# Kernel tuning notes

Hardware: AMD Instinct MI355X
Metric: run time of the kernel (lower is better)

Reference implementation:

```python
import jax, jax.numpy as jnp
import numpy as np

SCALE = 0.125          # feature stride 8
OUT = 7                # roi_align output size
SR = 2                 # sampling_ratio
BBW = (10.0, 10.0, 5.0, 5.0)   # torchvision BoxCoder weights
CLAMP = float(np.log(1000.0 / 16.0))
IMG_H, IMG_W = 800.0, 1088.0


def _bilinear(img, ys, xs):
    # img [C,H,W]; ys,xs [P] -> [C,P]
    C, H, W = img.shape
    y = jnp.clip(ys, 0.0, H - 1.0)
    x = jnp.clip(xs, 0.0, W - 1.0)
    y0 = jnp.floor(y); x0 = jnp.floor(x)
    y0i = y0.astype(jnp.int32); x0i = x0.astype(jnp.int32)
    y1i = jnp.minimum(y0i + 1, H - 1); x1i = jnp.minimum(x0i + 1, W - 1)
    ly = y - y0; lx = x - x0
    flat = img.reshape(C, H * W)
    g = lambda yi, xi: flat[:, yi * W + xi]
    return (g(y0i, x0i) * (1 - ly) * (1 - lx) + g(y0i, x1i) * (1 - ly) * lx
            + g(y1i, x0i) * ly * (1 - lx) + g(y1i, x1i) * ly * lx)


def _roi_align(features, boxes, roi_batch):
    # features [B,C,H,W], boxes [N,4] (image coords), roi_batch [N] -> [N,C,7,7]
    B, C, H, W = features.shape
    P = OUT * SR

    def one(b, box):
        x1, y1, x2, y2 = box[0] * SCALE, box[1] * SCALE, box[2] * SCALE, box[3] * SCALE
        rw = jnp.maximum(x2 - x1, 1.0)
        rh = jnp.maximum(y2 - y1, 1.0)
        bw = rw / OUT; bh = rh / OUT
        off = (jnp.arange(OUT)[:, None] + (jnp.arange(SR)[None, :] + 0.5) / SR).reshape(-1)  # [P]
        ys = y1 + off * bh
        xs = x1 + off * bw
        yy = jnp.repeat(ys, P)   # [P*P], y-major
        xx = jnp.tile(xs, P)
        v = _bilinear(features[b], yy, xx)                   # [C, P*P]
        return v.reshape(C, OUT, SR, OUT, SR).mean(axis=(2, 4))  # avg over samples

    return jax.vmap(one)(roi_batch, boxes)


def _decode(deltas, boxes):
    # deltas [N,K,4], boxes [N,4] -> [N,K,4]
    pw = boxes[:, 2] - boxes[:, 0]
    ph = boxes[:, 3] - boxes[:, 1]
    cx = boxes[:, 0] + 0.5 * pw
    cy = boxes[:, 1] + 0.5 * ph
    dx = deltas[..., 0] / BBW[0]; dy = deltas[..., 1] / BBW[1]
    dw = jnp.minimum(deltas[..., 2] / BBW[2], CLAMP)
    dh = jnp.minimum(deltas[..., 3] / BBW[3], CLAMP)
    pcx = dx * pw[:, None] + cx[:, None]
    pcy = dy * ph[:, None] + cy[:, None]
    pww = jnp.exp(dw) * pw[:, None]
    phh = jnp.exp(dh) * ph[:, None]
    out = jnp.stack([
        jnp.clip(pcx - 0.5 * pww, 0.0, IMG_W),
        jnp.clip(pcy - 0.5 * phh, 0.0, IMG_H),
        jnp.clip(pcx + 0.5 * pww, 0.0, IMG_W),
        jnp.clip(pcy + 0.5 * phh, 0.0, IMG_H),
    ], axis=-1)
    return out


def setup_inputs() -> dict:
    key = jax.random.key(0)
    ks = jax.random.split(key, 12)
    B, C, H, W, N, NC = 2, 256, 100, 136, 1000, 2
    features = jax.random.normal(ks[0], (B, C, H, W), jnp.float32)
    # valid proposal boxes in image coords
    cx = jax.random.uniform(ks[1], (N,)) * IMG_W
    cy = jax.random.uniform(ks[2], (N,)) * IMG_H
    bw = jax.random.uniform(ks[3], (N,)) * 240.0 + 16.0
    bh = jax.random.uniform(ks[4], (N,)) * 240.0 + 16.0
    x1 = jnp.clip(cx - 0.5 * bw, 0.0, IMG_W - 2.0)
    y1 = jnp.clip(cy - 0.5 * bh, 0.0, IMG_H - 2.0)
    x2 = jnp.clip(x1 + bw, x1 + 1.0, IMG_W - 1.0)
    y2 = jnp.clip(y1 + bh, y1 + 1.0, IMG_H - 1.0)
    boxes = jnp.stack([x1, y1, x2, y2], axis=-1).astype(jnp.float32)
    roi_batch = jax.random.randint(ks[5], (N,), 0, B, dtype=jnp.int32)
    D = C * OUT * OUT  # 12544
    HID = 1024
    s = 0.02
    fc1_w = jax.random.normal(ks[6], (D, HID), jnp.float32) * s
    fc1_b = jnp.zeros((HID,), jnp.float32)
    fc2_w = jax.random.normal(ks[7], (HID, HID), jnp.float32) * s
    fc2_b = jnp.zeros((HID,), jnp.float32)
    cls_w = jax.random.normal(ks[8], (HID, NC), jnp.float32) * s
    cls_b = jnp.zeros((NC,), jnp.float32)
    bbox_w = jax.random.normal(ks[9], (HID, NC * 4), jnp.float32) * s
    bbox_b = jnp.zeros((NC * 4,), jnp.float32)
    return {"features": features, "boxes": boxes, "roi_batch": roi_batch,
            "fc1_w": fc1_w, "fc1_b": fc1_b, "fc2_w": fc2_w, "fc2_b": fc2_b,
            "cls_w": cls_w, "cls_b": cls_b, "bbox_w": bbox_w, "bbox_b": bbox_b}


def reference(features, boxes, roi_batch, fc1_w, fc1_b, fc2_w, fc2_b, cls_w, cls_b, bbox_w, bbox_b):
    N = boxes.shape[0]
    feats = _roi_align(features, boxes, roi_batch).reshape(N, -1)  # [N, 12544]
    h = jax.nn.relu(feats @ fc1_w + fc1_b)                         # TwoMLPHead fc6
    h = jax.nn.relu(h @ fc2_w + fc2_b)                             # TwoMLPHead fc7
    scores = jax.nn.softmax(h @ cls_w + cls_b, axis=-1)            # [N, 2]
    deltas = (h @ bbox_w + bbox_b).reshape(N, -1, 4)               # [N, 2, 4]
    dec = _decode(deltas, boxes).reshape(N, -1)                    # [N, 8]
    return jnp.concatenate([dec, scores], axis=-1)                 # [N, 10]
```

## Files before the change

### kernel.cpp

```cpp
#include <hip/hip_runtime.h>
#include <hip/hip_bf16.h>

#define BF16 __hip_bfloat16

typedef __bf16 bf16x8 __attribute__((ext_vector_type(8)));
typedef float floatx4 __attribute__((ext_vector_type(4)));
typedef int intx4 __attribute__((ext_vector_type(4)));

__global__ __launch_bounds__(256) void transpose_all(const float* __restrict__ features,
                                                     const float* __restrict__ fc1_w,
                                                     const float* __restrict__ fc2_w,
                                                     BF16* __restrict__ featT,
                                                     BF16* __restrict__ w1t,
                                                     BF16* __restrict__ w2t) {
    __shared__ float tile[32][33];
    int bid = blockIdx.x;
    const float* ip;
    BF16* op;
    int R, C, cx, cy;
    if (bid < 6800) {
        int z = bid / 3400, r = bid - z * 3400;
        cx = r % 425; cy = r / 425;
        R = 256; C = 13600;
        ip = features + (size_t)z * 256 * 13600;
        op = featT + (size_t)z * 256 * 13600;
    } else if (bid < 19344) {
        int r = bid - 6800;
        cx = r & 31; cy = r >> 5;
        R = 12544; C = 1024;
        ip = fc1_w; op = w1t;
    } else {
        int r = bid - 19344;
        cx = r & 31; cy = r >> 5;
        R = 1024; C = 1024;
        ip = fc2_w; op = w2t;
    }
    int tx = threadIdx.x & 31, ty = threadIdx.x >> 5;
    int r0 = cy << 5, c0 = cx << 5;
#pragma unroll
    for (int i = 0; i < 4; ++i)
        tile[ty + i * 8][tx] = ip[(size_t)(r0 + ty + i * 8) * C + c0 + tx];
    __syncthreads();
#pragma unroll
    for (int i = 0; i < 4; ++i)
        op[(size_t)(c0 + ty + i * 8) * R + r0 + tx] = __float2bfloat16(tile[tx][ty + i * 8]);
}

__global__ __launch_bounds__(256) void roi_align_k(const BF16* __restrict__ featT,
                                                   const float* __restrict__ boxes,
                                                   const int* __restrict__ roi_batch,
                                                   BF16* __restrict__ feats) {
    __shared__ __align__(16) int   s_off[196][4];
    __shared__ __align__(16) float s_w[196][4];
    __shared__ BF16 lbuf[12544];
    int roi = blockIdx.x;
    int t = threadIdx.x;
    BF16* orow = feats + (size_t)roi * 12544;
    if (roi >= 1000) {
        uint4* o4 = (uint4*)orow;
        uint4 z = {0u, 0u, 0u, 0u};
        for (int i = t; i < 1568; i += 256) o4[i] = z;
        return;
    }
    int b = roi_batch[roi];

    if (t < 196) {
        float x1 = boxes[roi * 4 + 0] * 0.125f;
        float y1 = boxes[roi * 4 + 1] * 0.125f;
        float x2 = boxes[roi * 4 + 2] * 0.125f;
        float y2 = boxes[roi * 4 + 3] * 0.125f;
        float bw = fmaxf(x2 - x1, 1.0f) * (1.0f / 7.0f);
        float bh = fmaxf(y2 - y1, 1.0f) * (1.0f / 7.0f);
        int cell = t >> 2, s = t & 3;
        int oy = cell / 7, ox = cell - oy * 7;
        int sy = s >> 1, sx = s & 1;
        float yc = y1 + ((float)oy + ((float)sy + 0.5f) * 0.5f) * bh;
        float xc = x1 + ((float)ox + ((float)sx + 0.5f) * 0.5f) * bw;
        yc = fminf(fmaxf(yc, 0.0f), 99.0f);
        xc = fminf(fmaxf(xc, 0.0f), 135.0f);
        float y0f = floorf(yc), x0f = floorf(xc);
        int y0 = (int)y0f, x0 = (int)x0f;
        int y1i = min(y0 + 1, 99), x1i = min(x0 + 1, 135);
        float ly = yc - y0f, lx = xc - x0f;
        s_w[t][0] = (1.0f - ly) * (1.0f - lx) * 0.25f;
        s_w[t][1] = (1.0f - ly) * lx * 0.25f;
        s_w[t][2] = ly * (1.0f - lx) * 0.25f;
        s_w[t][3] = ly * lx * 0.25f;
        s_off[t][0] = (y0 * 136 + x0) * 256;
        s_off[t][1] = (y0 * 136 + x1i) * 256;
        s_off[t][2] = (y1i * 136 + x0) * 256;
        s_off[t][3] = (y1i * 136 + x1i) * 256;
    }
    __syncthreads();

    int cb = t & 31, g = t >> 5;
    const BF16* fb = featT + (size_t)b * (100 * 136 * 256) + cb * 8;
    int chbase = cb * 8;
    for (int cell = g; cell < 49; cell += 8) {
        float a[8];
#pragma unroll
        for (int j = 0; j < 8; ++j) a[j] = 0.0f;
#pragma unroll
        for (int s = 0; s < 4; ++s) {
            int p = cell * 4 + s;
#pragma unroll
            for (int tap = 0; tap < 4; ++tap) {
                float w = s_w[p][tap];
                bf16x8 v = *(const bf16x8*)(fb + s_off[p][tap]);
#pragma unroll
                for (int j = 0; j < 8; ++j) a[j] += w * (float)v[j];
            }
        }
#pragma unroll
        for (int j = 0; j < 8; ++j)
            lbuf[(chbase + j) * 49 + cell] = __float2bfloat16(a[j]);
    }
    __syncthreads();
    uint4* o4 = (uint4*)orow;
    const uint4* l4 = (const uint4*)lbuf;
    for (int i = t; i < 1568; i += 256) o4[i] = l4[i];
}

__global__ __launch_bounds__(256) void gemm_splitk(const BF16* __restrict__ A,
                                                   const BF16* __restrict__ Bt,
                                                   float* __restrict__ P,
                                                   int K, int chunk) {
    __shared__ char lds[2][2][16384];
    int w = threadIdx.x >> 6, l = threadIdx.x & 63;
    int wm = w & 1, wn = w >> 1;
    int tm = blockIdx.y, tn = blockIdx.x, s = blockIdx.z;
    int k0 = s * chunk;

    floatx4 acc[4][4];
#pragma unroll
    for (int i = 0; i < 4; ++i)
#pragma unroll
        for (int j = 0; j < 4; ++j) acc[i][j] = (floatx4){0.f, 0.f, 0.f, 0.f};

    const size_t strideA = (size_t)K * 2;
    int r8 = l >> 3;
    int g8 = (l & 7) ^ r8;
    const char* gA = (const char*)A + (size_t)(tm * 128 + w * 32 + r8) * strideA
                     + (size_t)k0 * 2 + (size_t)g8 * 16;
    const char* gB = (const char*)Bt + (size_t)(tn * 128 + w * 32 + r8) * strideA
                     + (size_t)k0 * 2 + (size_t)g8 * 16;
    int lw = w * 4096 + l * 16;

    int c = l & 15, q = l >> 4;
    int xa0 = ((0 * 4 + q) ^ (c & 7)) * 16;
    int xa1 = ((1 * 4 + q) ^ (c & 7)) * 16;
    int abase = (wm * 64 + c) * 128;
    int bbase = (wn * 64 + c) * 128;

    int nIter = chunk >> 6;

    intx4 pa[4], pb[4];
#pragma unroll
    for (int i = 0; i < 4; ++i) {
        pa[i] = *(const intx4*)(gA + (size_t)(i * 8) * strideA);
        pb[i] = *(const intx4*)(gB + (size_t)(i * 8) * strideA);
    }
#pragma unroll
    for (int i = 0; i < 4; ++i) {
        *(intx4*)(&lds[0][0][lw + i * 1024]) = pa[i];
        *(intx4*)(&lds[0][1][lw + i * 1024]) = pb[i];
    }
    __syncthreads();

    for (int kb = 0; kb < nIter; ++kb) {
        int cur = kb & 1;
        bool more = (kb + 1 < nIter);
        if (more) {
            size_t ko = (size_t)(kb + 1) * 128;
#pragma unroll
            for (int i = 0; i < 4; ++i) {
                pa[i] = *(const intx4*)(gA + (size_t)(i * 8) * strideA + ko);
                pb[i] = *(const intx4*)(gB + (size_t)(i * 8) * strideA + ko);
            }
        }
        const char* bufA = lds[cur][0];
        const char* bufB = lds[cur][1];
#pragma unroll
        for (int kk = 0; kk < 2; ++kk) {
            int xo = kk ? xa1 : xa0;
            bf16x8 af[4], bfr[4];
#pragma unroll
            for (int mi = 0; mi < 4; ++mi) af[mi] = *(const bf16x8*)(bufA + abase + mi * 2048 + xo);
#pragma unroll
            for (int ni = 0; ni < 4; ++ni) bfr[ni] = *(const bf16x8*)(bufB + bbase + ni * 2048 + xo);
#pragma unroll
            for (int mi = 0; mi < 4; ++mi)
#pragma unroll
                for (int ni = 0; ni < 4; ++ni)
                    acc[mi][ni] = __builtin_amdgcn_mfma_f32_16x16x32_bf16(af[mi], bfr[ni], acc[mi][ni], 0, 0, 0);
        }
        if (more) {
            char* nA = &lds[cur ^ 1][0][lw];
            char* nB = &lds[cur ^ 1][1][lw];
#pragma unroll
            for (int i = 0; i < 4; ++i) {
                *(intx4*)(nA + i * 1024) = pa[i];
                *(intx4*)(nB + i * 1024) = pb[i];
            }
        }
        __syncthreads();
    }

    size_t base = (size_t)s << 20;
#pragma unroll
    for (int mi = 0; mi < 4; ++mi) {
        int rowG = tm * 128 + wm * 64 + mi * 16 + q * 4;
#pragma unroll
        for (int ni = 0; ni < 4; ++ni) {
            int colG = tn * 128 + wn * 64 + ni * 16 + c;
#pragma unroll
            for (int r = 0; r < 4; ++r)
                P[base + (size_t)(rowG + r) * 1024 + colG] = acc[mi][ni][r];
        }
    }
}

__global__ __launch_bounds__(256) void reduce_k(const float* __restrict__ P,
                                                const float* __restrict__ bias,
                                                BF16* __restrict__ out,
                                                int S) {
    int i = blockIdx.x * 256 + threadIdx.x;
    float a = bias[i & 1023];
    for (int s = 0; s < S; ++s) a += P[((size_t)s << 20) + i];
    a = fmaxf(a, 0.0f);
    out[i] = __float2bfloat16(a);
}

__global__ __launch_bounds__(256) void head_k(const float* __restrict__ P2,
                                              const float* __restrict__ fc2_b,
                                              const float* __restrict__ cls_w,
                                              const float* __restrict__ cls_b,
                                              const float* __restrict__ bbox_w,
                                              const float* __restrict__ bbox_b,
                                              const float* __restrict__ boxes,
                                              float* __restrict__ out, int S2) {
    __shared__ float red[4][10];
    int roi = blockIdx.x;
    int t = threadIdx.x, w = t >> 6, l = t & 63;
    int k4 = t * 4;

    floatx4 h = *(const floatx4*)(fc2_b + k4);
    const float* pbase = P2 + (size_t)roi * 1024 + k4;
    for (int s = 0; s < S2; ++s) {
        floatx4 p = *(const floatx4*)(pbase + ((size_t)s << 20));
        h.x += p.x; h.y += p.y; h.z += p.z; h.w += p.w;
    }
    h.x = fmaxf(h.x, 0.f); h.y = fmaxf(h.y, 0.f); h.z = fmaxf(h.z, 0.f); h.w = fmaxf(h.w, 0.f);

    float acc[10];
#pragma unroll
    for (int j = 0; j < 10; ++j) acc[j] = 0.0f;
    floatx4 c0 = *(const floatx4*)(cls_w + k4 * 2);
    floatx4 c1 = *(const floatx4*)(cls_w + k4 * 2 + 4);
    acc[0] = h.x * c0.x + h.y * c0.z + h.z * c1.x + h.w * c1.z;
    acc[1] = h.x * c0.y + h.y * c0.w + h.z * c1.y + h.w * c1.w;
    const float* bw = bbox_w + k4 * 8;
#pragma unroll
    for (int kk = 0; kk < 4; ++kk) {
        float hv = (kk == 0) ? h.x : (kk == 1) ? h.y : (kk == 2) ? h.z : h.w;
        floatx4 b0 = *(const floatx4*)(bw + kk * 8);
        floatx4 b1 = *(const floatx4*)(bw + kk * 8 + 4);
        acc[2] += hv * b0.x; acc[3] += hv * b0.y; acc[4] += hv * b0.z; acc[5] += hv * b0.w;
        acc[6] += hv * b1.x; acc[7] += hv * b1.y; acc[8] += hv * b1.z; acc[9] += hv * b1.w;
    }
#pragma unroll
    for (int j = 0; j < 10; ++j) {
#pragma unroll
        for (int off = 32; off > 0; off >>= 1) acc[j] += __shfl_down(acc[j], off);
    }
    if (l == 0) {
#pragma unroll
        for (int j = 0; j < 10; ++j) red[w][j] = acc[j];
    }
    __syncthreads();
    if (t == 0) {
        float f[10];
#pragma unroll
        for (int j = 0; j < 10; ++j) f[j] = red[0][j] + red[1][j] + red[2][j] + red[3][j];
        float s0 = f[0] + cls_b[0], s1 = f[1] + cls_b[1];
        float m = fmaxf(s0, s1);
        float e0 = expf(s0 - m), e1 = expf(s1 - m);
        float inv = 1.0f / (e0 + e1);

        float bx1 = boxes[roi * 4 + 0], by1 = boxes[roi * 4 + 1];
        float bx2 = boxes[roi * 4 + 2], by2 = boxes[roi * 4 + 3];
        float pw = bx2 - bx1, ph = by2 - by1;
        float cx = bx1 + 0.5f * pw, cy = by1 + 0.5f * ph;
        const float CLAMPV = 4.135166556742356f;
        float* orow = out + roi * 10;
#pragma unroll
        for (int cl = 0; cl < 2; ++cl) {
            float dx = (f[2 + cl * 4 + 0] + bbox_b[cl * 4 + 0]) * 0.1f;
            float dy = (f[2 + cl * 4 + 1] + bbox_b[cl * 4 + 1]) * 0.1f;
            float dw = fminf((f[2 + cl * 4 + 2] + bbox_b[cl * 4 + 2]) * 0.2f, CLAMPV);
            float dh = fminf((f[2 + cl * 4 + 3] + bbox_b[cl * 4 + 3]) * 0.2f, CLAMPV);
            float pcx = dx * pw + cx, pcy = dy * ph + cy;
            float pww = expf(dw) * pw, phh = expf(dh) * ph;
            orow[cl * 4 + 0] = fminf(fmaxf(pcx - 0.5f * pww, 0.0f), 1088.0f);
            orow[cl * 4 + 1] = fminf(fmaxf(pcy - 0.5f * phh, 0.0f), 800.0f);
            orow[cl * 4 + 2] = fminf(fmaxf(pcx + 0.5f * pww, 0.0f), 1088.0f);
            orow[cl * 4 + 3] = fminf(fmaxf(pcy + 0.5f * phh, 0.0f), 800.0f);
        }
        orow[8] = e0 * inv;
        orow[9] = e1 * inv;
    }
}

extern "C" void kernel_launch(void* const* d_in, const int* in_sizes, int n_in,
                              void* d_out, int out_size, void* d_ws, size_t ws_size,
                              hipStream_t stream) {
    const float* features = (const float*)d_in[0];
    const float* boxes    = (const float*)d_in[1];
    const int*   roi_b    = (const int*)d_in[2];
    const float* fc1_w    = (const float*)d_in[3];
    const float* fc1_b    = (const float*)d_in[4];
    const float* fc2_w    = (const float*)d_in[5];
    const float* fc2_b    = (const float*)d_in[6];
    const float* cls_w    = (const float*)d_in[7];
    const float* cls_b    = (const float*)d_in[8];
    const float* bbox_w   = (const float*)d_in[9];
    const float* bbox_b   = (const float*)d_in[10];
    float* out = (float*)d_out;

    char* ws = (char*)d_ws;
    BF16* featT = (BF16*)(ws + 0);
    BF16* w1t   = (BF16*)(ws + 13926400);
    BF16* w2t   = (BF16*)(ws + 39616512);
    BF16* feats = (BF16*)(ws + 41713664);
    BF16* h1    = (BF16*)(ws + 67403776);
    float* P1   = (float*)(ws + 69500928);
    float* P2   = (float*)(ws + 0);

    int S1 = 7;
    int S2 = 4;

    transpose_all<<<20368, 256, 0, stream>>>(features, fc1_w, fc2_w, featT, w1t, w2t);

    roi_align_k<<<1024, 256, 0, stream>>>(featT, boxes, roi_b, feats);

    gemm_splitk<<<dim3(8, 8, S1), 256, 0, stream>>>(feats, w1t, P1, 12544, 12544 / S1);
    reduce_k<<<4096, 256, 0, stream>>>(P1, fc1_b, h1, S1);

    gemm_splitk<<<dim3(8, 8, S2), 256, 0, stream>>>(h1, w2t, P2, 1024, 1024 / S2);

    head_k<<<1000, 256, 0, stream>>>(P2, fc2_b, cls_w, cls_b, bbox_w, bbox_b, boxes, out, S2);
}
```

Baseline: 216.0 us.

## Widen GEMM tiles to 128x256, raise split-K, fold weight transposes into ROI kernel

The split-K GEMM now computes a 128x256 output tile per block, using 32 accumulator fragments per wave and one LDS buffer instead of two, with an extra barrier per k-step. Split-K depth doubles (14 for fc6, 8 for fc7) and the grid is flattened to one dimension. The weight transposes move out of the feature-transpose kernel and into the ROI-align launch as extra blocks, so they can run alongside the ROI gathers. The wider tiles are meant to improve operand reuse and MFMA density, but they add register pressure and double the partial-sum buffer that the reduction must read.

```diff
diff --git a/kernel.cpp b/kernel.cpp
--- a/kernel.cpp
+++ b/kernel.cpp
@@ -7,34 +7,15 @@
 typedef float floatx4 __attribute__((ext_vector_type(4)));
 typedef int intx4 __attribute__((ext_vector_type(4)));
 
-__global__ __launch_bounds__(256) void transpose_all(const float* __restrict__ features,
-                                                     const float* __restrict__ fc1_w,
-                                                     const float* __restrict__ fc2_w,
-                                                     BF16* __restrict__ featT,
-                                                     BF16* __restrict__ w1t,
-                                                     BF16* __restrict__ w2t) {
+__global__ __launch_bounds__(256) void transpose_feat(const float* __restrict__ features,
+                                                      BF16* __restrict__ featT) {
     __shared__ float tile[32][33];
     int bid = blockIdx.x;
-    const float* ip;
-    BF16* op;
-    int R, C, cx, cy;
-    if (bid < 6800) {
-        int z = bid / 3400, r = bid - z * 3400;
-        cx = r % 425; cy = r / 425;
-        R = 256; C = 13600;
-        ip = features + (size_t)z * 256 * 13600;
-        op = featT + (size_t)z * 256 * 13600;
-    } else if (bid < 19344) {
-        int r = bid - 6800;
-        cx = r & 31; cy = r >> 5;
-        R = 12544; C = 1024;
-        ip = fc1_w; op = w1t;
-    } else {
-        int r = bid - 19344;
-        cx = r & 31; cy = r >> 5;
-        R = 1024; C = 1024;
-        ip = fc2_w; op = w2t;
-    }
+    int z = bid / 3400, r = bid - z * 3400;
+    int cx = r % 425, cy = r / 425;
+    const int R = 256, C = 13600;
+    const float* ip = features + (size_t)z * R * C;
+    BF16* op = featT + (size_t)z * R * C;
     int tx = threadIdx.x & 31, ty = threadIdx.x >> 5;
     int r0 = cy << 5, c0 = cx << 5;
 #pragma unroll
@@ -46,15 +27,49 @@
         op[(size_t)(c0 + ty + i * 8) * R + r0 + tx] = __float2bfloat16(tile[tx][ty + i * 8]);
 }
 
-__global__ __launch_bounds__(256) void roi_align_k(const BF16* __restrict__ featT,
-                                                   const float* __restrict__ boxes,
-                                                   const int* __restrict__ roi_batch,
-                                                   BF16* __restrict__ feats) {
+__global__ __launch_bounds__(256) void roi_and_wt(const BF16* __restrict__ featT,
+                                                  const float* __restrict__ boxes,
+                                                  const int* __restrict__ roi_batch,
+                                                  BF16* __restrict__ feats,
+                                                  const float* __restrict__ fc1_w,
+                                                  const float* __restrict__ fc2_w,
+                                                  BF16* __restrict__ w1t,
+                                                  BF16* __restrict__ w2t) {
     __shared__ __align__(16) int   s_off[196][4];
     __shared__ __align__(16) float s_w[196][4];
     __shared__ BF16 lbuf[12544];
-    int roi = blockIdx.x;
+    int bid = blockIdx.x;
     int t = threadIdx.x;
+
+    if (bid >= 1024) {
+        float (*tile)[33] = (float (*)[33])lbuf;
+        int r = bid - 1024;
+        const float* ip;
+        BF16* op;
+        int R, C, cx, cy;
+        if (r < 12544) {
+            cx = r & 31; cy = r >> 5;
+            R = 12544; C = 1024;
+            ip = fc1_w; op = w1t;
+        } else {
+            int r2 = r - 12544;
+            cx = r2 & 31; cy = r2 >> 5;
+            R = 1024; C = 1024;
+            ip = fc2_w; op = w2t;
+        }
+        int tx = t & 31, ty = t >> 5;
+        int r0 = cy << 5, c0 = cx << 5;
+#pragma unroll
+        for (int i = 0; i < 4; ++i)
+            tile[ty + i * 8][tx] = ip[(size_t)(r0 + ty + i * 8) * C + c0 + tx];
+        __syncthreads();
+#pragma unroll
+        for (int i = 0; i < 4; ++i)
+            op[(size_t)(c0 + ty + i * 8) * R + r0 + tx] = __float2bfloat16(tile[tx][ty + i * 8]);
+        return;
+    }
+
+    int roi = bid;
     BF16* orow = feats + (size_t)roi * 12544;
     if (roi >= 1000) {
         uint4* o4 = (uint4*)orow;
@@ -125,83 +140,77 @@
                                                    const BF16* __restrict__ Bt,
                                                    float* __restrict__ P,
                                                    int K, int chunk) {
-    __shared__ char lds[2][2][16384];
+    __shared__ char lds[49152];
     int w = threadIdx.x >> 6, l = threadIdx.x & 63;
     int wm = w & 1, wn = w >> 1;
-    int tm = blockIdx.y, tn = blockIdx.x, s = blockIdx.z;
+    int lin = blockIdx.x;
+    int tn = lin & 3, tm = (lin >> 2) & 7, s = lin >> 5;
     int k0 = s * chunk;
 
-    floatx4 acc[4][4];
+    floatx4 acc[4][8];
 #pragma unroll
     for (int i = 0; i < 4; ++i)
 #pragma unroll
-        for (int j = 0; j < 4; ++j) acc[i][j] = (floatx4){0.f, 0.f, 0.f, 0.f};
+        for (int j = 0; j < 8; ++j) acc[i][j] = (floatx4){0.f, 0.f, 0.f, 0.f};
 
     const size_t strideA = (size_t)K * 2;
     int r8 = l >> 3;
     int g8 = (l & 7) ^ r8;
     const char* gA = (const char*)A + (size_t)(tm * 128 + w * 32 + r8) * strideA
                      + (size_t)k0 * 2 + (size_t)g8 * 16;
-    const char* gB = (const char*)Bt + (size_t)(tn * 128 + w * 32 + r8) * strideA
+    const char* gB = (const char*)Bt + (size_t)(tn * 256 + w * 64 + r8) * strideA
                      + (size_t)k0 * 2 + (size_t)g8 * 16;
-    int lw = w * 4096 + l * 16;
+    int lwA = w * 4096 + l * 16;
+    int lwB = 16384 + w * 8192 + l * 16;
 
     int c = l & 15, q = l >> 4;
-    int xa0 = ((0 * 4 + q) ^ (c & 7)) * 16;
-    int xa1 = ((1 * 4 + q) ^ (c & 7)) * 16;
+    int xo0 = ((0 * 4 + q) ^ (c & 7)) * 16;
+    int xo1 = ((1 * 4 + q) ^ (c & 7)) * 16;
     int abase = (wm * 64 + c) * 128;
-    int bbase = (wn * 64 + c) * 128;
+    int bbase = 16384 + (wn * 128 + c) * 128;
 
     int nIter = chunk >> 6;
 
-    intx4 pa[4], pb[4];
-#pragma unroll
-    for (int i = 0; i < 4; ++i) {
-        pa[i] = *(const intx4*)(gA + (size_t)(i * 8) * strideA);
-        pb[i] = *(const intx4*)(gB + (size_t)(i * 8) * strideA);
-    }
-#pragma unroll
-    for (int i = 0; i < 4; ++i) {
-        *(intx4*)(&lds[0][0][lw + i * 1024]) = pa[i];
-        *(intx4*)(&lds[0][1][lw + i * 1024]) = pb[i];
-    }
+    intx4 ra[4], rb[8];
+#pragma unroll
+    for (int i = 0; i < 4; ++i) ra[i] = *(const intx4*)(gA + (size_t)(i * 8) * strideA);
+#pragma unroll
+    for (int i = 0; i < 8; ++i) rb[i] = *(const intx4*)(gB + (size_t)(i * 8) * strideA);
+#pragma unroll
+    for (int i = 0; i < 4; ++i) *(intx4*)(&lds[lwA + i * 1024]) = ra[i];
+#pragma unroll
+    for (int i = 0; i < 8; ++i) *(intx4*)(&lds[lwB + i * 1024]) = rb[i];
     __syncthreads();
 
     for (int kb = 0; kb < nIter; ++kb) {
-        int cur = kb & 1;
         bool more = (kb + 1 < nIter);
         if (more) {
             size_t ko = (size_t)(kb + 1) * 128;
 #pragma unroll
-            for (int i = 0; i < 4; ++i) {
-                pa[i] = *(const intx4*)(gA + (size_t)(i * 8) * strideA + ko);
-                pb[i] = *(const intx4*)(gB + (size_t)(i * 8) * strideA + ko);
-            }
-        }
-        const char* bufA = lds[cur][0];
-        const char* bufB = lds[cur][1];
+            for (int i = 0; i < 4; ++i) ra[i] = *(const intx4*)(gA + (size_t)(i * 8) * strideA + ko);
+#pragma unroll
+            for (int i = 0; i < 8; ++i) rb[i] = *(const intx4*)(gB + (size_t)(i * 8) * strideA + ko);
+        }
 #pragma unroll
         for (int kk = 0; kk < 2; ++kk) {
-            int xo = kk ? xa1 : xa0;
-            bf16x8 af[4], bfr[4];
-#pragma unroll
-            for (int mi = 0; mi < 4; ++mi) af[mi] = *(const bf16x8*)(bufA + abase + mi * 2048 + xo);
-#pragma unroll
-            for (int ni = 0; ni < 4; ++ni) bfr[ni] = *(const bf16x8*)(bufB + bbase + ni * 2048 + xo);
+            int xo = kk ? xo1 : xo0;
+            bf16x8 af[4], bfr[8];
+#pragma unroll
+            for (int mi = 0; mi < 4; ++mi) af[mi] = *(const bf16x8*)(&lds[abase + mi * 2048 + xo]);
+#pragma unroll
+            for (int ni = 0; ni < 8; ++ni) bfr[ni] = *(const bf16x8*)(&lds[bbase + ni * 2048 + xo]);
 #pragma unroll
             for (int mi = 0; mi < 4; ++mi)
 #pragma unroll
-                for (int ni = 0; ni < 4; ++ni)
+                for (int ni = 0; ni < 8; ++ni)
                     acc[mi][ni] = __builtin_amdgcn_mfma_f32_16x16x32_bf16(af[mi], bfr[ni], acc[mi][ni], 0, 0, 0);
         }
+        __syncthreads();
         if (more) {
-            char* nA = &lds[cur ^ 1][0][lw];
-            char* nB = &lds[cur ^ 1][1][lw];
-#pragma unroll
-            for (int i = 0; i < 4; ++i) {
-                *(intx4*)(nA + i * 1024) = pa[i];
-                *(intx4*)(nB + i * 1024) = pb[i];
-            }
+#pragma unroll
+            for (int i = 0; i < 4; ++i) *(intx4*)(&lds[lwA + i * 1024]) = ra[i];
+#pragma unroll
+            for (int i = 0; i < 8; ++i) *(intx4*)(&lds[lwB + i * 1024]) = rb[i];
         }
         __syncthreads();
     }
@@ -211,8 +220,8 @@
     for (int mi = 0; mi < 4; ++mi) {
         int rowG = tm * 128 + wm * 64 + mi * 16 + q * 4;
 #pragma unroll
-        for (int ni = 0; ni < 4; ++ni) {
-            int colG = tn * 128 + wn * 64 + ni * 16 + c;
+        for (int ni = 0; ni < 8; ++ni) {
+            int colG = tn * 256 + wn * 128 + ni * 16 + c;
 #pragma unroll
             for (int r = 0; r < 4; ++r)
                 P[base + (size_t)(rowG + r) * 1024 + colG] = acc[mi][ni][r];
@@ -336,17 +345,18 @@
     float* P1   = (float*)(ws + 69500928);
     float* P2   = (float*)(ws + 0);
 
-    int S1 = 7;
-    int S2 = 4;
-
-    transpose_all<<<20368, 256, 0, stream>>>(features, fc1_w, fc2_w, featT, w1t, w2t);
-
-    roi_align_k<<<1024, 256, 0, stream>>>(featT, boxes, roi_b, feats);
-
-    gemm_splitk<<<dim3(8, 8, S1), 256, 0, stream>>>(feats, w1t, P1, 12544, 12544 / S1);
+    int S1 = 14;
+    int S2 = 8;
+
+    transpose_feat<<<6800, 256, 0, stream>>>(features, featT);
+
+    roi_and_wt<<<1024 + 12544 + 1024, 256, 0, stream>>>(featT, boxes, roi_b, feats,
+                                                        fc1_w, fc2_w, w1t, w2t);
+
+    gemm_splitk<<<32 * S1, 256, 0, stream>>>(feats, w1t, P1, 12544, 12544 / S1);
     reduce_k<<<4096, 256, 0, stream>>>(P1, fc1_b, h1, S1);
 
-    gemm_splitk<<<dim3(8, 8, S2), 256, 0, stream>>>(h1, w2t, P2, 1024, 1024 / S2);
+    gemm_splitk<<<32 * S2, 256, 0, stream>>>(h1, w2t, P2, 1024, 1024 / S2);
 
     head_k<<<1000, 256, 0, stream>>>(P2, fc2_b, cls_w, cls_b, bbox_w, bbox_b, boxes, out, S2);
 }
```

New measurement: 228.4 us. +5.8%, slower.
